# Kernel tuning notes

Hardware: AMD Instinct MI355X
Metric: run time of the kernel (lower is better)

## Reference

```python
import jax, jax.numpy as jnp
import numpy as np

EPS = 1e-12  # F.normalize default eps


def setup_inputs() -> dict:
    key = jax.random.key(0)
    k1, k2 = jax.random.split(key)
    b, c, angRes, h, w = 4, 64, 5, 64, 64
    d = 64  # dims
    x = jax.random.normal(k1, (b, c, angRes * angRes, h, w), dtype=jnp.float32)
    # 1x1 conv weight [3*dims, channels] (kernel size 1, no bias)
    W = jax.random.normal(k2, (3 * d, c), dtype=jnp.float32) * 0.02
    return {"x": x, "W": W}


def reference(x, W):
    b, c, n, h, w = x.shape
    d = W.shape[0] // 3
    # 1x1 conv over angular (u,v) grid == channel matmul; rearranges are free reindexings
    qkv = jnp.einsum('oc,bcnhw->bonhw', W, x)  # [b, 3d, n, h, w]
    q, k, v = jnp.split(qkv, 3, axis=1)        # each [b, d, n, h, w]

    def flat(t):  # '(b h w) c u v -> b (u v) (c h w)'
        return t.transpose(0, 2, 1, 3, 4).reshape(b, n, d * h * w)

    q, k, v = flat(q), flat(k), flat(v)
    # L2-normalize along the (c h w) feature dim (k was normalized on dim=-2 of its
    # transposed layout, which is this same feature dim)
    q = q / jnp.maximum(jnp.linalg.norm(q, axis=-1, keepdims=True), EPS)
    k = k / jnp.maximum(jnp.linalg.norm(k, axis=-1, keepdims=True), EPS)
    att = jax.nn.softmax(jnp.einsum('bnf,bmf->bnm', q, k), axis=-1)  # [b, n, n], n=25
    out = jnp.einsum('bnm,bmf->bnf', att, v)   # [b, n, d*h*w]
    # 'b (u v) (c h w) -> b c (u v) h w'
    return out.reshape(b, n, d, h, w).transpose(0, 2, 1, 3, 4)
```

## Files before the change

### kernel.cpp

```cpp
#include <hip/hip_runtime.h>

#define B   4
#define C   64
#define D   64
#define NN  25
#define HW  4096
#define F   (D*HW)

#define SW  256
#define PT  128

typedef unsigned short ushort_t;
typedef unsigned int   uint_t;
typedef __attribute__((ext_vector_type(8)))  short  short8;
typedef __attribute__((ext_vector_type(16))) float  floatx16;
typedef __attribute__((ext_vector_type(4)))  float  f32x4;
typedef __attribute__((ext_vector_type(4)))  unsigned short us4;

__device__ ushort_t g_Wthi[128 * C];
__device__ ushort_t g_Wtlo[128 * C];
__device__ ushort_t g_Wvhi[D * C];
__device__ ushort_t g_Wvlo[D * C];

static __device__ __forceinline__ ushort_t f2bf(float f) {
    uint_t u = __float_as_uint(f);
    u += 0x7FFFu + ((u >> 16) & 1u);
    return (ushort_t)(u >> 16);
}
static __device__ __forceinline__ float bf2f(ushort_t h) {
    return __uint_as_float((uint_t)h << 16);
}

static __device__ __forceinline__ int lds_x(int p, int c) {
    return p * 64 + ((((c >> 3) ^ (p & 7)) << 3) | (c & 7));
}

__global__ void k_zero(float* acc) {
    int i = blockIdx.x * 256 + threadIdx.x;
    if (i < 2700) acc[i] = 0.f;
}

__global__ void k_wprep(const float* __restrict__ W) {
    int i = blockIdx.x * 256 + threadIdx.x;
    if (i < 128 * 64) {
        float w = W[i];
        ushort_t hi = f2bf(w);
        g_Wthi[i] = hi;
        g_Wtlo[i] = f2bf(w - bf2f(hi));
    } else if (i < 192 * 64) {
        float w = W[i];
        int j = i - 128 * 64;
        ushort_t hi = f2bf(w);
        g_Wvhi[j] = hi;
        g_Wvlo[j] = f2bf(w - bf2f(hi));
    }
}

__global__ void __launch_bounds__(256, 4)
k_qkmfma(const float* __restrict__ x,
         ushort_t* __restrict__ Q, ushort_t* __restrict__ K,
         float* __restrict__ qq, float* __restrict__ kk) {
    __shared__ ushort_t sXhi[PT * 64];
    __shared__ ushort_t sXlo[PT * 64];

    const int t  = threadIdx.x;
    const int wv = t >> 6, ln = t & 63;
    const int n  = blockIdx.y, b = blockIdx.z;
    const int gp0 = blockIdx.x * PT;

    const int row = ln & 31, kh = (ln >> 5) * 8, d0 = wv * 32;
    short8 ahi[4], alo[4];
#pragma unroll
    for (int ks = 0; ks < 4; ++ks) {
        ahi[ks] = *(const short8*)&g_Wthi[(d0 + row) * 64 + ks * 16 + kh];
        alo[ks] = *(const short8*)&g_Wtlo[(d0 + row) * 64 + ks * 16 + kh];
    }

    {
        const int c16 = wv * 16;
#pragma unroll
        for (int cg = 0; cg < 4; ++cg) {
            const int c4 = c16 + cg * 4;
            const float* xc = x + ((size_t)(b * C + c4) * NN + n) * HW + gp0;
#pragma unroll
            for (int ph = 0; ph < 2; ++ph) {
                const int p = ph * 64 + ln;
                float v[4];
#pragma unroll
                for (int i = 0; i < 4; ++i) v[i] = xc[(size_t)i * NN * HW + p];
                us4 h, l;
#pragma unroll
                for (int i = 0; i < 4; ++i) {
                    ushort_t hi = f2bf(v[i]);
                    h[i] = hi;
                    l[i] = f2bf(v[i] - bf2f(hi));
                }
                *(us4*)&sXhi[lds_x(p, c4)] = h;
                *(us4*)&sXlo[lds_x(p, c4)] = l;
            }
        }
    }
    __syncthreads();

    ushort_t* __restrict__ O = (wv < 2) ? Q : K;
    const int dbase = (wv < 2) ? d0 : (d0 - 64);
    const size_t obase = ((size_t)(b * NN + n) * D + dbase) * HW + gp0;

    float nrm = 0.f;
#pragma unroll
    for (int pt = 0; pt < 4; ++pt) {
        const int pcol = pt * 32 + row;
        floatx16 acc;
#pragma unroll
        for (int r = 0; r < 16; ++r) acc[r] = 0.f;
#pragma unroll
        for (int ks = 0; ks < 4; ++ks) {
            const int c0 = ks * 16 + kh;
            short8 bhi = *(const short8*)&sXhi[lds_x(pcol, c0)];
            short8 blo = *(const short8*)&sXlo[lds_x(pcol, c0)];
            acc = __builtin_amdgcn_mfma_f32_32x32x16_bf16(ahi[ks], bhi, acc, 0, 0, 0);
            acc = __builtin_amdgcn_mfma_f32_32x32x16_bf16(alo[ks], bhi, acc, 0, 0, 0);
            acc = __builtin_amdgcn_mfma_f32_32x32x16_bf16(ahi[ks], blo, acc, 0, 0, 0);
        }
#pragma unroll
        for (int r = 0; r < 16; ++r) {
            const int dr = (r & 3) + 8 * (r >> 2) + 4 * (ln >> 5);
            nrm += acc[r] * acc[r];
            O[obase + (size_t)dr * HW + pcol] = f2bf(acc[r]);
        }
    }
    for (int off = 32; off > 0; off >>= 1) nrm += __shfl_xor(nrm, off);
    if (ln == 0) atomicAdd(((wv < 2) ? qq : kk) + b * NN + n, nrm);
}

__global__ void k_sqk(const ushort_t* __restrict__ Q, const ushort_t* __restrict__ K,
                      float* __restrict__ S) {
    const int t  = threadIdx.x;
    const int wv = t >> 6, ln = t & 63;
    const int b  = blockIdx.y;
    const int row  = ln & 31;
    const int rowc = (row < NN) ? row : (NN - 1);
    const int kh   = (ln >> 5) * 8;
    const size_t f0 = (size_t)blockIdx.x * (4 * SW) + (size_t)wv * SW;
    const ushort_t* Qp = Q + ((size_t)b * NN + rowc) * F + f0 + kh;
    const ushort_t* Kp = K + ((size_t)b * NN + rowc) * F + f0 + kh;

    floatx16 acc;
#pragma unroll
    for (int r = 0; r < 16; ++r) acc[r] = 0.f;

    for (int s = 0; s < SW / 16; ++s) {
        short8 aq = *(const short8*)(Qp + s * 16);
        short8 bk = *(const short8*)(Kp + s * 16);
        acc = __builtin_amdgcn_mfma_f32_32x32x16_bf16(aq, bk, acc, 0, 0, 0);
    }

    __shared__ float redS[4][64][17];
#pragma unroll
    for (int r = 0; r < 16; ++r) redS[wv][ln][r] = acc[r];
    __syncthreads();
    if (wv == 0) {
#pragma unroll
        for (int r = 0; r < 16; ++r) {
            float v = redS[0][ln][r] + redS[1][ln][r] + redS[2][ln][r] + redS[3][ln][r];
            const int srow = (r & 3) + 8 * (r >> 2) + 4 * (ln >> 5);
            const int scol = ln & 31;
            if (srow < NN && scol < NN)
                atomicAdd(&S[((size_t)b * NN + srow) * NN + scol], v);
        }
    }
}

__global__ void k_softmax(const float* __restrict__ S, const float* __restrict__ qq,
                          const float* __restrict__ kk, float* __restrict__ attT) {
    const int b = blockIdx.x, n = threadIdx.x;
    if (n >= NN) return;
    const float qn = fmaxf(sqrtf(qq[b * NN + n]), 1e-12f);
    float l[NN], mx = -1e30f;
#pragma unroll
    for (int m = 0; m < NN; ++m) {
        const float km = fmaxf(sqrtf(kk[b * NN + m]), 1e-12f);
        l[m] = S[((size_t)b * NN + n) * NN + m] / (qn * km);
        mx = fmaxf(mx, l[m]);
    }
    float s = 0.f;
#pragma unroll
    for (int m = 0; m < NN; ++m) { l[m] = expf(l[m] - mx); s += l[m]; }
    const float inv = 1.f / s;
#pragma unroll
    for (int m = 0; m < NN; ++m) attT[((size_t)b * NN + m) * NN + n] = l[m] * inv;
}

__global__ void __launch_bounds__(256, 4)
k_mix(const float* __restrict__ x, const float* __restrict__ attT,
      float* __restrict__ xa) {
    const int p = (blockIdx.x * 256 + threadIdx.x) * 4;
    const int c = blockIdx.y, b = blockIdx.z;
    const float* xb = x + ((size_t)(b * C + c) * NN) * HW + p;
    const float* at = attT + (size_t)b * NN * NN;
    f32x4 acc[NN];
#pragma unroll
    for (int n = 0; n < NN; ++n) acc[n] = 0.f;
#pragma unroll 5
    for (int m = 0; m < NN; ++m) {
        const f32x4 xm = *(const f32x4*)(xb + (size_t)m * HW);
#pragma unroll
        for (int n = 0; n < NN; ++n) acc[n] += at[m * NN + n] * xm;
    }
#pragma unroll
    for (int n = 0; n < NN; ++n)
        *(f32x4*)&xa[((size_t)(b * C + c) * NN + n) * HW + p] = acc[n];
}

__global__ void __launch_bounds__(256, 4)
k_vproj(const float* __restrict__ xa, float* __restrict__ out) {
    __shared__ ushort_t sXhi[PT * 64];
    __shared__ ushort_t sXlo[PT * 64];

    const int t  = threadIdx.x;
    const int wv = t >> 6, ln = t & 63;
    const int n  = blockIdx.y, b = blockIdx.z;
    const int gp0 = blockIdx.x * PT;

    const int row = ln & 31, kh = (ln >> 5) * 8;
    const int d0  = (wv & 1) * 32;
    short8 ahi[4], alo[4];
#pragma unroll
    for (int ks = 0; ks < 4; ++ks) {
        ahi[ks] = *(const short8*)&g_Wvhi[(d0 + row) * 64 + ks * 16 + kh];
        alo[ks] = *(const short8*)&g_Wvlo[(d0 + row) * 64 + ks * 16 + kh];
    }

    {
        const int c16 = wv * 16;
#pragma unroll
        for (int cg = 0; cg < 4; ++cg) {
            const int c4 = c16 + cg * 4;
            const float* xc = xa + ((size_t)(b * C + c4) * NN + n) * HW + gp0;
#pragma unroll
            for (int ph = 0; ph < 2; ++ph) {
                const int p = ph * 64 + ln;
                float v[4];
#pragma unroll
                for (int i = 0; i < 4; ++i) v[i] = xc[(size_t)i * NN * HW + p];
                us4 h, l;
#pragma unroll
                for (int i = 0; i < 4; ++i) {
                    ushort_t hi = f2bf(v[i]);
                    h[i] = hi;
                    l[i] = f2bf(v[i] - bf2f(hi));
                }
                *(us4*)&sXhi[lds_x(p, c4)] = h;
                *(us4*)&sXlo[lds_x(p, c4)] = l;
            }
        }
    }
    __syncthreads();

    const int ph0 = (wv >> 1) * 64;
#pragma unroll
    for (int pt = 0; pt < 2; ++pt) {
        const int pcol = ph0 + pt * 32 + row;
        floatx16 acc;
#pragma unroll
        for (int r = 0; r < 16; ++r) acc[r] = 0.f;
#pragma unroll
        for (int ks = 0; ks < 4; ++ks) {
            const int c0 = ks * 16 + kh;
            short8 bhi = *(const short8*)&sXhi[lds_x(pcol, c0)];
            short8 blo = *(const short8*)&sXlo[lds_x(pcol, c0)];
            acc = __builtin_amdgcn_mfma_f32_32x32x16_bf16(ahi[ks], bhi, acc, 0, 0, 0);
            acc = __builtin_amdgcn_mfma_f32_32x32x16_bf16(alo[ks], bhi, acc, 0, 0, 0);
            acc = __builtin_amdgcn_mfma_f32_32x32x16_bf16(ahi[ks], blo, acc, 0, 0, 0);
        }
#pragma unroll
        for (int r = 0; r < 16; ++r) {
            const int dr = (r & 3) + 8 * (r >> 2) + 4 * (ln >> 5);
            out[((size_t)(b * D + d0 + dr) * NN + n) * HW + gp0 + pcol] = acc[r];
        }
    }
}

extern "C" void kernel_launch(void* const* d_in, const int* in_sizes, int n_in,
                              void* d_out, int out_size, void* d_ws, size_t ws_size,
                              hipStream_t stream) {
    const float* x = (const float*)d_in[0];
    const float* W = (const float*)d_in[1];
    float* outf = (float*)d_out;

    ushort_t* Q  = (ushort_t*)d_ws;
    ushort_t* K  = Q + (size_t)B * NN * F;
    float*    xa = (float*)d_ws;

    float* S    = outf;
    float* qq   = outf + 2500;
    float* kk   = outf + 2600;
    float* attT = outf + 2700;

    k_zero   <<<dim3(11),             256, 0, stream>>>(outf);
    k_wprep  <<<dim3(48),             256, 0, stream>>>(W);
    k_qkmfma <<<dim3(HW/PT, NN, B),   256, 0, stream>>>(x, Q, K, qq, kk);
    k_sqk    <<<dim3(F/(4*SW), B),    256, 0, stream>>>(Q, K, S);
    k_softmax<<<dim3(B),               64, 0, stream>>>(S, qq, kk, attT);
    k_mix    <<<dim3(HW/1024, C, B),  256, 0, stream>>>(x, attT, xa);
    k_vproj  <<<dim3(HW/PT, NN, B),   256, 0, stream>>>(xa, outf);
}
```

Before: 315.6 us.

## Fuse V projection into QK projection and mix attention over projected V

The Q, K and V projections now run in one kernel that reads x once, with V written in a fragment-native layout to the workspace. The attention mix then works on V and scatters straight to the output, which removes the separate mixed-x buffer and the second x-sized projection pass. Q and K are stored in the MFMA fragment order with vectorized stores and staged in the output buffer, and the small reduction buffers move to device globals. The cost is an fp32 V intermediate and scattered scalar stores in the final kernel.

```diff
diff --git a/kernel.cpp b/kernel.cpp
--- a/kernel.cpp
+++ b/kernel.cpp
@@ -22,6 +22,11 @@
 __device__ ushort_t g_Wvhi[D * C];
 __device__ ushort_t g_Wvlo[D * C];
 
+__device__ float g_S[B * NN * NN];
+__device__ float g_qq[B * NN];
+__device__ float g_kk[B * NN];
+__device__ float g_attT[B * NN * NN];
+
 static __device__ __forceinline__ ushort_t f2bf(float f) {
     uint_t u = __float_as_uint(f);
     u += 0x7FFFu + ((u >> 16) & 1u);
@@ -35,9 +40,11 @@
     return p * 64 + ((((c >> 3) ^ (p & 7)) << 3) | (c & 7));
 }
 
-__global__ void k_zero(float* acc) {
+__global__ void k_zero() {
     int i = blockIdx.x * 256 + threadIdx.x;
-    if (i < 2700) acc[i] = 0.f;
+    if (i < 2500)      g_S[i] = 0.f;
+    else if (i < 2600) g_qq[i - 2500] = 0.f;
+    else if (i < 2700) g_kk[i - 2600] = 0.f;
 }
 
 __global__ void k_wprep(const float* __restrict__ W) {
@@ -57,16 +64,17 @@
 }
 
 __global__ void __launch_bounds__(256, 4)
-k_qkmfma(const float* __restrict__ x,
-         ushort_t* __restrict__ Q, ushort_t* __restrict__ K,
-         float* __restrict__ qq, float* __restrict__ kk) {
+k_proj(const float* __restrict__ x,
+       ushort_t* __restrict__ Q, ushort_t* __restrict__ K,
+       float* __restrict__ V) {
     __shared__ ushort_t sXhi[PT * 64];
     __shared__ ushort_t sXlo[PT * 64];
 
     const int t  = threadIdx.x;
     const int wv = t >> 6, ln = t & 63;
     const int n  = blockIdx.y, b = blockIdx.z;
-    const int gp0 = blockIdx.x * PT;
+    const int tile = blockIdx.x;
+    const int gp0  = tile * PT;
 
     const int row = ln & 31, kh = (ln >> 5) * 8, d0 = wv * 32;
     short8 ahi[4], alo[4];
@@ -103,8 +111,8 @@
     __syncthreads();
 
     ushort_t* __restrict__ O = (wv < 2) ? Q : K;
-    const int dbase = (wv < 2) ? d0 : (d0 - 64);
-    const size_t obase = ((size_t)(b * NN + n) * D + dbase) * HW + gp0;
+    const int slab = (wv < 2) ? wv : wv - 2;
+    const size_t nbase = (size_t)(b * NN + n) * F;
 
     float nrm = 0.f;
 #pragma unroll
@@ -123,18 +131,59 @@
             acc = __builtin_amdgcn_mfma_f32_32x32x16_bf16(ahi[ks], blo, acc, 0, 0, 0);
         }
 #pragma unroll
-        for (int r = 0; r < 16; ++r) {
-            const int dr = (r & 3) + 8 * (r >> 2) + 4 * (ln >> 5);
-            nrm += acc[r] * acc[r];
-            O[obase + (size_t)dr * HW + pcol] = f2bf(acc[r]);
+        for (int r4 = 0; r4 < 4; ++r4) {
+            us4 h;
+#pragma unroll
+            for (int j = 0; j < 4; ++j) {
+                const float a = acc[r4 * 4 + j];
+                nrm += a * a;
+                h[j] = f2bf(a);
+            }
+            *(us4*)&O[nbase + (((size_t)((tile * 2 + slab) * 16 + pt * 4 + r4)) << 8)
+                      + ln * 4] = h;
         }
     }
     for (int off = 32; off > 0; off >>= 1) nrm += __shfl_xor(nrm, off);
-    if (ln == 0) atomicAdd(((wv < 2) ? qq : kk) + b * NN + n, nrm);
-}
-
-__global__ void k_sqk(const ushort_t* __restrict__ Q, const ushort_t* __restrict__ K,
-                      float* __restrict__ S) {
+    if (ln == 0) atomicAdd(((wv < 2) ? g_qq : g_kk) + b * NN + n, nrm);
+
+    {
+        const int sv = wv & 1, ph = wv >> 1;
+        short8 vhi[4], vlo[4];
+#pragma unroll
+        for (int ks = 0; ks < 4; ++ks) {
+            vhi[ks] = *(const short8*)&g_Wvhi[(sv * 32 + row) * 64 + ks * 16 + kh];
+            vlo[ks] = *(const short8*)&g_Wvlo[(sv * 32 + row) * 64 + ks * 16 + kh];
+        }
+#pragma unroll
+        for (int pt = 0; pt < 2; ++pt) {
+            const int pcol = ph * 64 + pt * 32 + row;
+            floatx16 acc;
+#pragma unroll
+            for (int r = 0; r < 16; ++r) acc[r] = 0.f;
+#pragma unroll
+            for (int ks = 0; ks < 4; ++ks) {
+                const int c0 = ks * 16 + kh;
+                short8 bhi = *(const short8*)&sXhi[lds_x(pcol, c0)];
+                short8 blo = *(const short8*)&sXlo[lds_x(pcol, c0)];
+                acc = __builtin_amdgcn_mfma_f32_32x32x16_bf16(vhi[ks], bhi, acc, 0, 0, 0);
+                acc = __builtin_amdgcn_mfma_f32_32x32x16_bf16(vlo[ks], bhi, acc, 0, 0, 0);
+                acc = __builtin_amdgcn_mfma_f32_32x32x16_bf16(vhi[ks], blo, acc, 0, 0, 0);
+            }
+#pragma unroll
+            for (int r4 = 0; r4 < 4; ++r4) {
+                f32x4 o;
+#pragma unroll
+                for (int j = 0; j < 4; ++j) o[j] = acc[r4 * 4 + j];
+                V[nbase + (((size_t)((((tile * 2 + sv) * 2 + ph) * 2 + pt) * 4 + r4)) << 8)
+                  + ln * 4] = o[0],
+                *(f32x4*)&V[nbase + (((size_t)((((tile * 2 + sv) * 2 + ph) * 2 + pt) * 4
+                  + r4)) << 8) + ln * 4] = o;
+            }
+        }
+    }
+}
+
+__global__ void k_sqk(const ushort_t* __restrict__ Q, const ushort_t* __restrict__ K) {
     const int t  = threadIdx.x;
     const int wv = t >> 6, ln = t & 63;
     const int b  = blockIdx.y;
@@ -166,21 +215,20 @@
             const int srow = (r & 3) + 8 * (r >> 2) + 4 * (ln >> 5);
             const int scol = ln & 31;
             if (srow < NN && scol < NN)
-                atomicAdd(&S[((size_t)b * NN + srow) * NN + scol], v);
-        }
-    }
-}
-
-__global__ void k_softmax(const float* __restrict__ S, const float* __restrict__ qq,
-                          const float* __restrict__ kk, float* __restrict__ attT) {
+                atomicAdd(&g_S[((size_t)b * NN + srow) * NN + scol], v);
+        }
+    }
+}
+
+__global__ void k_softmax() {
     const int b = blockIdx.x, n = threadIdx.x;
     if (n >= NN) return;
-    const float qn = fmaxf(sqrtf(qq[b * NN + n]), 1e-12f);
+    const float qn = fmaxf(sqrtf(g_qq[b * NN + n]), 1e-12f);
     float l[NN], mx = -1e30f;
 #pragma unroll
     for (int m = 0; m < NN; ++m) {
-        const float km = fmaxf(sqrtf(kk[b * NN + m]), 1e-12f);
-        l[m] = S[((size_t)b * NN + n) * NN + m] / (qn * km);
+        const float km = fmaxf(sqrtf(g_kk[b * NN + m]), 1e-12f);
+        l[m] = g_S[((size_t)b * NN + n) * NN + m] / (qn * km);
         mx = fmaxf(mx, l[m]);
     }
     float s = 0.f;
@@ -188,97 +236,36 @@
     for (int m = 0; m < NN; ++m) { l[m] = expf(l[m] - mx); s += l[m]; }
     const float inv = 1.f / s;
 #pragma unroll
-    for (int m = 0; m < NN; ++m) attT[((size_t)b * NN + m) * NN + n] = l[m] * inv;
+    for (int m = 0; m < NN; ++m) g_attT[((size_t)b * NN + m) * NN + n] = l[m] * inv;
 }
 
 __global__ void __launch_bounds__(256, 4)
-k_mix(const float* __restrict__ x, const float* __restrict__ attT,
-      float* __restrict__ xa) {
-    const int p = (blockIdx.x * 256 + threadIdx.x) * 4;
-    const int c = blockIdx.y, b = blockIdx.z;
-    const float* xb = x + ((size_t)(b * C + c) * NN) * HW + p;
-    const float* at = attT + (size_t)b * NN * NN;
+k_outmix(const float* __restrict__ V, float* __restrict__ out) {
+    const int tid = blockIdx.x * 256 + threadIdx.x;
+    const int b   = blockIdx.y;
+    const float* Vb = V + (size_t)b * NN * F + (size_t)tid * 4;
+    const float* at = g_attT + b * NN * NN;
+
     f32x4 acc[NN];
 #pragma unroll
     for (int n = 0; n < NN; ++n) acc[n] = 0.f;
 #pragma unroll 5
     for (int m = 0; m < NN; ++m) {
-        const f32x4 xm = *(const f32x4*)(xb + (size_t)m * HW);
-#pragma unroll
-        for (int n = 0; n < NN; ++n) acc[n] += at[m * NN + n] * xm;
-    }
+        const f32x4 v = *(const f32x4*)(Vb + (size_t)m * F);
+#pragma unroll
+        for (int n = 0; n < NN; ++n) acc[n] += at[m * NN + n] * v;
+    }
+
+    const int ln = tid & 63, c0 = tid >> 6;
+    const int r4 = c0 & 3, pt = (c0 >> 2) & 1, ph = (c0 >> 3) & 1;
+    const int sv = (c0 >> 4) & 1, tile = c0 >> 5;
+    const int p  = tile * 128 + ph * 64 + pt * 32 + (ln & 31);
+    const int db = sv * 32 + 8 * r4 + 4 * (ln >> 5);
 #pragma unroll
     for (int n = 0; n < NN; ++n)
-        *(f32x4*)&xa[((size_t)(b * C + c) * NN + n) * HW + p] = acc[n];
-}
-
-__global__ void __launch_bounds__(256, 4)
-k_vproj(const float* __restrict__ xa, float* __restrict__ out) {
-    __shared__ ushort_t sXhi[PT * 64];
-    __shared__ ushort_t sXlo[PT * 64];
-
-    const int t  = threadIdx.x;
-    const int wv = t >> 6, ln = t & 63;
-    const int n  = blockIdx.y, b = blockIdx.z;
-    const int gp0 = blockIdx.x * PT;
-
-    const int row = ln & 31, kh = (ln >> 5) * 8;
-    const int d0  = (wv & 1) * 32;
-    short8 ahi[4], alo[4];
-#pragma unroll
-    for (int ks = 0; ks < 4; ++ks) {
-        ahi[ks] = *(const short8*)&g_Wvhi[(d0 + row) * 64 + ks * 16 + kh];
-        alo[ks] = *(const short8*)&g_Wvlo[(d0 + row) * 64 + ks * 16 + kh];
-    }
-
-    {
-        const int c16 = wv * 16;
-#pragma unroll
-        for (int cg = 0; cg < 4; ++cg) {
-            const int c4 = c16 + cg * 4;
-            const float* xc = xa + ((size_t)(b * C + c4) * NN + n) * HW + gp0;
-#pragma unroll
-            for (int ph = 0; ph < 2; ++ph) {
-                const int p = ph * 64 + ln;
-                float v[4];
-#pragma unroll
-                for (int i = 0; i < 4; ++i) v[i] = xc[(size_t)i * NN * HW + p];
-                us4 h, l;
-#pragma unroll
-                for (int i = 0; i < 4; ++i) {
-                    ushort_t hi = f2bf(v[i]);
-                    h[i] = hi;
-                    l[i] = f2bf(v[i] - bf2f(hi));
-                }
-                *(us4*)&sXhi[lds_x(p, c4)] = h;
-                *(us4*)&sXlo[lds_x(p, c4)] = l;
-            }
-        }
-    }
-    __syncthreads();
-
-    const int ph0 = (wv >> 1) * 64;
-#pragma unroll
-    for (int pt = 0; pt < 2; ++pt) {
-        const int pcol = ph0 + pt * 32 + row;
-        floatx16 acc;
-#pragma unroll
-        for (int r = 0; r < 16; ++r) acc[r] = 0.f;
-#pragma unroll
-        for (int ks = 0; ks < 4; ++ks) {
-            const int c0 = ks * 16 + kh;
-            short8 bhi = *(const short8*)&sXhi[lds_x(pcol, c0)];
-            short8 blo = *(const short8*)&sXlo[lds_x(pcol, c0)];
-            acc = __builtin_amdgcn_mfma_f32_32x32x16_bf16(ahi[ks], bhi, acc, 0, 0, 0);
-            acc = __builtin_amdgcn_mfma_f32_32x32x16_bf16(alo[ks], bhi, acc, 0, 0, 0);
-            acc = __builtin_amdgcn_mfma_f32_32x32x16_bf16(ahi[ks], blo, acc, 0, 0, 0);
-        }
-#pragma unroll
-        for (int r = 0; r < 16; ++r) {
-            const int dr = (r & 3) + 8 * (r >> 2) + 4 * (ln >> 5);
-            out[((size_t)(b * D + d0 + dr) * NN + n) * HW + gp0 + pcol] = acc[r];
-        }
-    }
+#pragma unroll
+        for (int j = 0; j < 4; ++j)
+            out[((size_t)(b * D + db + j) * NN + n) * HW + p] = acc[n][j];
 }
 
 extern "C" void kernel_launch(void* const* d_in, const int* in_sizes, int n_in,
@@ -288,20 +275,14 @@
     const float* W = (const float*)d_in[1];
     float* outf = (float*)d_out;
 
-    ushort_t* Q  = (ushort_t*)d_ws;
-    ushort_t* K  = Q + (size_t)B * NN * F;
-    float*    xa = (float*)d_ws;
-
-    float* S    = outf;
-    float* qq   = outf + 2500;
-    float* kk   = outf + 2600;
-    float* attT = outf + 2700;
-
-    k_zero   <<<dim3(11),             256, 0, stream>>>(outf);
-    k_wprep  <<<dim3(48),             256, 0, stream>>>(W);
-    k_qkmfma <<<dim3(HW/PT, NN, B),   256, 0, stream>>>(x, Q, K, qq, kk);
-    k_sqk    <<<dim3(F/(4*SW), B),    256, 0, stream>>>(Q, K, S);
-    k_softmax<<<dim3(B),               64, 0, stream>>>(S, qq, kk, attT);
-    k_mix    <<<dim3(HW/1024, C, B),  256, 0, stream>>>(x, attT, xa);
-    k_vproj  <<<dim3(HW/PT, NN, B),   256, 0, stream>>>(xa, outf);
-}
+    ushort_t* Q = (ushort_t*)d_out;
+    ushort_t* K = Q + (size_t)B * NN * F;
+    float*    V = (float*)d_ws;
+
+    k_zero   <<<dim3(11),           256, 0, stream>>>();
+    k_wprep  <<<dim3(48),           256, 0, stream>>>(W);
+    k_proj   <<<dim3(HW/PT, NN, B), 256, 0, stream>>>(x, Q, K, V);
+    k_sqk    <<<dim3(F/(4*SW), B),  256, 0, stream>>>(Q, K);
+    k_softmax<<<dim3(B),             64, 0, stream>>>();
+    k_outmix <<<dim3(F/1024, B),    256, 0, stream>>>(V, outf);
+}
```

New measurement: 309.7 us. About the same (-1.9%).
